# Optimization experiments

Measured on AMD Instinct MI355X. Metric: run time of the kernel, lower is better.

Reference implementation:

```python
import jax, jax.numpy as jnp
import numpy as np

B, S, H, NH = 2, 2048, 2048, 16
HD = H // NH  # 128
ROPE_BASE = 10000.0


def rotate_half(x):
    x1, x2 = x[..., : x.shape[-1] // 2], x[..., x.shape[-1] // 2 :]
    return jnp.concatenate((-x2, x1), axis=-1)


def rope_cos_sin(seq_len, dim, dtype):
    inv_freq = 1.0 / (ROPE_BASE ** (jnp.arange(0, dim, 2, dtype=jnp.float32) / dim))
    t = jnp.arange(seq_len, dtype=jnp.float32)
    freqs = jnp.einsum('i,j->ij', t, inv_freq)          # [S, dim/2]
    emb = jnp.concatenate((freqs, freqs), axis=-1)       # [S, dim]
    return jnp.cos(emb).astype(dtype), jnp.sin(emb).astype(dtype)


def setup_inputs() -> dict:
    key = jax.random.key(0)
    ks = jax.random.split(key, 5)
    std = 1.0 / np.sqrt(H)
    return {
        'hidden_states': jax.random.normal(ks[0], (B, S, H), dtype=jnp.float32),
        'Wq': jax.random.normal(ks[1], (H, H), dtype=jnp.float32) * std,
        'Wk': jax.random.normal(ks[2], (H, H), dtype=jnp.float32) * std,
        'Wv': jax.random.normal(ks[3], (H, H), dtype=jnp.float32) * std,
        'Wo': jax.random.normal(ks[4], (H, H), dtype=jnp.float32) * std,
    }


def reference(hidden_states, Wq, Wk, Wv, Wo):
    bsz, q_len, _ = hidden_states.shape
    scale = 1.0 / np.sqrt(HD)
    # QKV projections (nn.Linear: x @ W.T)
    q = (hidden_states @ Wq.T).reshape(bsz, q_len, NH, HD).transpose(0, 2, 1, 3)
    k = (hidden_states @ Wk.T).reshape(bsz, q_len, NH, HD).transpose(0, 2, 1, 3)
    v = (hidden_states @ Wv.T).reshape(bsz, q_len, NH, HD).transpose(0, 2, 1, 3)
    # RoPE
    cos, sin = rope_cos_sin(q_len, HD, hidden_states.dtype)  # [S, HD]
    cos = cos[None, None]
    sin = sin[None, None]
    q = q * cos + rotate_half(q) * sin
    k = k * cos + rotate_half(k) * sin
    # attention (no mask, eval dropout = identity)
    attn = jnp.einsum('bhqd,bhkd->bhqk', q, k) * scale
    attn = jax.nn.softmax(attn.astype(jnp.float32), axis=-1).astype(q.dtype)
    out = jnp.einsum('bhqk,bhkd->bhqd', attn, v)
    out = out.transpose(0, 2, 1, 3).reshape(bsz, q_len, H)
    return out @ Wo.T
```

## Files before the change

kernel.cpp:

```cpp
#include <hip/hip_runtime.h>
#include <hip/hip_bf16.h>
#include <math.h>

#define Bb 2
#define Ss 2048
#define Hh 2048
#define NHh 16
#define HDd 128
#define Mm (Bb*Ss)

typedef __bf16 bf16;
typedef __bf16 bf16x8 __attribute__((ext_vector_type(8)));
typedef __bf16 bf16x4 __attribute__((ext_vector_type(4)));
typedef float  f32x4  __attribute__((ext_vector_type(4)));

#define MFMA16(a,b,c) __builtin_amdgcn_mfma_f32_16x16x32_bf16((a),(b),(c),0,0,0)

__device__ __forceinline__ void gll16(const void* g, void* l) {
  __builtin_amdgcn_global_load_lds((__attribute__((address_space(1))) void*)g,
                                   (__attribute__((address_space(3))) void*)l, 16, 0, 0);
}

__global__ __launch_bounds__(256) void k_tables(float* __restrict__ cosT, float* __restrict__ sinT) {
  int id = blockIdx.x * 256 + threadIdx.x;
  int s = id >> 6, j = id & 63;
  float inv = 1.0f / powf(10000.0f, (float)j * (1.0f/64.0f));
  float a = (float)s * inv;
  cosT[id] = cosf(a);
  sinT[id] = sinf(a);
}

__global__ __launch_bounds__(256) void k_cvt(const float* __restrict__ in, bf16* __restrict__ out) {
  size_t i = ((size_t)blockIdx.x * 256 + threadIdx.x) * 4;
  float4 v = *(const float4*)(in + i);
  bf16x4 r = { (bf16)v.x, (bf16)v.y, (bf16)v.z, (bf16)v.w };
  *(bf16x4*)(out + i) = r;
}

template<int EPI>
__global__ __launch_bounds__(256) void k_gemm(
    const bf16* __restrict__ A, const bf16* __restrict__ Bw,
    float* __restrict__ C, bf16* __restrict__ QKb, bf16* __restrict__ Vt,
    int M, int N, int K)
{
  __shared__ bf16 As[128*64];
  __shared__ bf16 Bs[128*64];
  const int tid = threadIdx.x;
  const int lane = tid & 63;
  const int w = tid >> 6, wm = w & 1, wn = w >> 1;
  const int cpx = gridDim.x >> 3;
  const int bid = (blockIdx.x & 7) * cpx + (blockIdx.x >> 3);
  const int mt = M >> 7;
  const int bm = bid % mt, bn = bid / mt;
  const int r8 = tid >> 3, c8 = tid & 7;
  const bf16* Ag = A  + (size_t)(bm*128 + r8) * K + c8*8;
  const bf16* Bg = Bw + (size_t)(bn*128 + r8) * K + c8*8;
  bf16* Asw = &As[r8*64 + c8*8];
  bf16* Bsw = &Bs[r8*64 + c8*8];

  f32x4 acc[4][4] = {};
  for (int k0 = 0; k0 < K; k0 += 64) {
#pragma unroll
    for (int i = 0; i < 4; ++i) {
      gll16(Ag + (size_t)i*32*K + k0, Asw + i*32*64);
      gll16(Bg + (size_t)i*32*K + k0, Bsw + i*32*64);
    }
    __syncthreads();
#pragma unroll
    for (int kc = 0; kc < 2; ++kc) {
      bf16x8 af[4], bfv[4];
#pragma unroll
      for (int mi = 0; mi < 4; ++mi)
        af[mi] = *(const bf16x8*)&As[(wm*64 + mi*16 + (lane & 15))*64 + kc*32 + (lane>>4)*8];
#pragma unroll
      for (int ni = 0; ni < 4; ++ni)
        bfv[ni] = *(const bf16x8*)&Bs[(wn*64 + ni*16 + (lane & 15))*64 + kc*32 + (lane>>4)*8];
#pragma unroll
      for (int mi = 0; mi < 4; ++mi)
#pragma unroll
        for (int ni = 0; ni < 4; ++ni)
          acc[mi][ni] = MFMA16(af[mi], bfv[ni], acc[mi][ni]);
    }
    __syncthreads();
  }
  const int colB = bn*128 + wn*64;
  if (EPI == 0) {
#pragma unroll
    for (int mi = 0; mi < 4; ++mi)
#pragma unroll
      for (int ni = 0; ni < 4; ++ni) {
        int row0 = bm*128 + wm*64 + mi*16 + (lane>>4)*4;
        int col  = colB + ni*16 + (lane & 15);
#pragma unroll
        for (int r = 0; r < 4; ++r)
          C[(size_t)(row0 + r) * N + col] = acc[mi][ni][r];
      }
  } else if (colB < 4096) {
#pragma unroll
    for (int mi = 0; mi < 4; ++mi)
#pragma unroll
      for (int ni = 0; ni < 4; ++ni) {
        int row0 = bm*128 + wm*64 + mi*16 + (lane>>4)*4;
        int col  = colB + ni*16 + (lane & 15);
#pragma unroll
        for (int r = 0; r < 4; ++r)
          QKb[(size_t)(row0 + r) * 4096 + col] = (bf16)acc[mi][ni][r];
      }
  } else {
#pragma unroll
    for (int mi = 0; mi < 4; ++mi)
#pragma unroll
      for (int ni = 0; ni < 4; ++ni) {
        int row0 = bm*128 + wm*64 + mi*16 + (lane>>4)*4;
        int n2   = colB + ni*16 + (lane & 15) - 4096;
        int b = row0 >> 11, s0 = row0 & (Ss-1);
        bf16x4 pk = { (bf16)acc[mi][ni][0], (bf16)acc[mi][ni][1],
                      (bf16)acc[mi][ni][2], (bf16)acc[mi][ni][3] };
        *(bf16x4*)&Vt[((size_t)(b*NHh + (n2>>7))*HDd + (n2&127))*Ss + s0] = pk;
      }
  }
}

__global__ __launch_bounds__(256) void k_rope(
    const bf16* __restrict__ QKb,
    const float* __restrict__ cosT, const float* __restrict__ sinT,
    bf16* __restrict__ Qb, bf16* __restrict__ Kb)
{
  const size_t id = (size_t)blockIdx.x * 256 + threadIdx.x;
  const int j = (int)(id & 63);
  const size_t row = id >> 6;
  const size_t tok = row >> 4;
  const int h = (int)(row & 15);
  const int s = (int)(tok & (Ss - 1));
  const float c = cosT[s*64 + j], sn = sinT[s*64 + j];
  const size_t qbase = tok * 4096 + h * 128;
  const float scale = 0.12753102543421936f;
  float q1 = (float)QKb[qbase + j],        q2 = (float)QKb[qbase + 64 + j];
  float k1 = (float)QKb[qbase + 2048 + j], k2 = (float)QKb[qbase + 2048 + 64 + j];
  const size_t obase = row * HDd;
  Qb[obase + j]      = (bf16)((q1*c - q2*sn) * scale);
  Qb[obase + 64 + j] = (bf16)((q2*c + q1*sn) * scale);
  Kb[obase + j]      = (bf16)(k1*c - k2*sn);
  Kb[obase + 64 + j] = (bf16)(k2*c + k1*sn);
}

__global__ __launch_bounds__(256) void k_attn(
    const bf16* __restrict__ Qb, const bf16* __restrict__ Kb,
    const bf16* __restrict__ Vt, bf16* __restrict__ Ob)
{
  __shared__ bf16 Ks[2][64*128];
  __shared__ bf16 Vs[2][128*64];
  __shared__ bf16 Ps[64*72];
  const int cpx = gridDim.x >> 3;
  const int blk = (blockIdx.x & 7) * cpx + (blockIdx.x >> 3);
  const int bh = blk >> 5;
  const int q0 = (blk & 31) * 64;
  const int b = bh >> 4, h = bh & 15;
  const int tid = threadIdx.x, lane = tid & 63, w = tid >> 6;

  const int rK = tid >> 4, cK = tid & 15;
  const int rV = tid >> 3, cV = tid & 7;
  const bf16* Kg0 = Kb + ((size_t)b*Ss*NHh + h) * HDd;
  const bf16* Vg0 = Vt + (size_t)bh * HDd * Ss;

  auto stage = [&](int bufi, int kv0) {
#pragma unroll
    for (int i = 0; i < 4; ++i) {
      const int rowK = i*16 + rK; const int sck = cK ^ (rowK & 7);
      gll16(Kg0 + (size_t)(kv0 + rowK)*(NHh*HDd) + sck*8, &Ks[bufi][rowK*128 + cK*8]);
      const int rowV = i*32 + rV; const int scv = cV ^ (rowV & 7);
      gll16(Vg0 + (size_t)rowV*Ss + kv0 + scv*8, &Vs[bufi][rowV*64 + cV*8]);
    }
  };

  bf16x8 aq[4];
  {
    const int qr = q0 + w*16 + (lane & 15);
    const bf16* qp = Qb + ((size_t)(b*Ss + qr) * NHh + h) * HDd + (lane>>4)*8;
#pragma unroll
    for (int kc = 0; kc < 4; ++kc) aq[kc] = *(const bf16x8*)(qp + kc*32);
  }
  float m_i[4], l_par[4];
  f32x4 o[8] = {};
#pragma unroll
  for (int i = 0; i < 4; ++i) { m_i[i] = -1e30f; l_par[i] = 0.f; }

  stage(0, 0);
  asm volatile("s_waitcnt vmcnt(0)" ::: "memory");
  __builtin_amdgcn_s_barrier();
  asm volatile("" ::: "memory");

  const int NT = Ss / 64;
  for (int t = 0; t < NT; ++t) {
    const int cur = t & 1;
    if (t + 1 < NT) stage(cur ^ 1, (t + 1) * 64);

    f32x4 sf[4];
    __builtin_amdgcn_s_setprio(1);
#pragma unroll
    for (int nf = 0; nf < 4; ++nf) {
      f32x4 a = {0.f,0.f,0.f,0.f};
#pragma unroll
      for (int kc = 0; kc < 4; ++kc) {
        const int row = nf*16 + (lane & 15);
        const int ch  = kc*4 + (lane>>4);
        bf16x8 bk = *(const bf16x8*)&Ks[cur][row*128 + (ch ^ (row & 7))*8];
        a = MFMA16(aq[kc], bk, a);
      }
      sf[nf] = a;
    }
    __builtin_amdgcn_s_setprio(0);

    float xl[4];
#pragma unroll
    for (int i = 0; i < 4; ++i)
      xl[i] = fmaxf(fmaxf(sf[0][i], sf[1][i]), fmaxf(sf[2][i], sf[3][i]));
    bool grow = (xl[0] > m_i[0] + 11.5f) || (xl[1] > m_i[1] + 11.5f) ||
                (xl[2] > m_i[2] + 11.5f) || (xl[3] > m_i[3] + 11.5f);
    if (__any(grow)) {
#pragma unroll
      for (int i = 0; i < 4; ++i) {
        float x = xl[i];
        x = fmaxf(x, __shfl_xor(x, 1));
        x = fmaxf(x, __shfl_xor(x, 2));
        x = fmaxf(x, __shfl_xor(x, 4));
        x = fmaxf(x, __shfl_xor(x, 8));
        float mnew = fmaxf(m_i[i], x);
        float c = exp2f(m_i[i] - mnew);
        m_i[i] = mnew; l_par[i] *= c;
#pragma unroll
        for (int nfo = 0; nfo < 8; ++nfo) o[nfo][i] *= c;
      }
    }
#pragma unroll
    for (int nf = 0; nf < 4; ++nf)
#pragma unroll
      for (int i = 0; i < 4; ++i) {
        float pv = exp2f(sf[nf][i] - m_i[i]);
        sf[nf][i] = pv;
        l_par[i] += pv;
      }
#pragma unroll
    for (int nf = 0; nf < 4; ++nf)
#pragma unroll
      for (int i = 0; i < 4; ++i)
        Ps[(w*16 + (lane>>4)*4 + i)*72 + nf*16 + (lane & 15)] = (bf16)sf[nf][i];

    __builtin_amdgcn_s_setprio(1);
#pragma unroll
    for (int kc = 0; kc < 2; ++kc) {
      bf16x8 pa = *(const bf16x8*)&Ps[(w*16 + (lane & 15))*72 + kc*32 + (lane>>4)*8];
#pragma unroll
      for (int nfo = 0; nfo < 8; ++nfo) {
        const int row = nfo*16 + (lane & 15);
        const int ch  = kc*4 + (lane>>4);
        bf16x8 bv = *(const bf16x8*)&Vs[cur][row*64 + (ch ^ (row & 7))*8];
        o[nfo] = MFMA16(pa, bv, o[nfo]);
      }
    }
    __builtin_amdgcn_s_setprio(0);

    asm volatile("s_waitcnt vmcnt(0)" ::: "memory");
    __builtin_amdgcn_s_barrier();
    asm volatile("" ::: "memory");
  }

  float linv[4];
#pragma unroll
  for (int i = 0; i < 4; ++i) {
    float s = l_par[i];
    s += __shfl_xor(s, 1); s += __shfl_xor(s, 2);
    s += __shfl_xor(s, 4); s += __shfl_xor(s, 8);
    linv[i] = 1.0f / s;
  }
#pragma unroll
  for (int nfo = 0; nfo < 8; ++nfo)
#pragma unroll
    for (int i = 0; i < 4; ++i) {
      const int qr = q0 + w*16 + (lane>>4)*4 + i;
      const int d  = nfo*16 + (lane & 15);
      Ob[((size_t)(b*Ss + qr) * NHh + h) * HDd + d] = (bf16)(o[nfo][i] * linv[i]);
    }
}

extern "C" void kernel_launch(void* const* d_in, const int* in_sizes, int n_in,
                              void* d_out, int out_size, void* d_ws, size_t ws_size,
                              hipStream_t stream) {
  (void)in_sizes; (void)n_in; (void)out_size; (void)ws_size;
  const float* X  = (const float*)d_in[0];
  const float* Wq = (const float*)d_in[1];
  const float* Wk = (const float*)d_in[2];
  const float* Wv = (const float*)d_in[3];
  const float* Wo = (const float*)d_in[4];
  float* out = (float*)d_out;

  char* p = (char*)d_ws;
  size_t off = 0;
  auto take = [&](size_t bytes) { char* r = p + off; off += (bytes + 255) & ~(size_t)255; return r; };

  float* cosT = (float*)take((size_t)Ss*64*4);
  float* sinT = (float*)take((size_t)Ss*64*4);
  bf16*  Xb   = (bf16*) take((size_t)Mm*Hh*2);
  bf16*  Wqkv = (bf16*) take((size_t)3*Hh*Hh*2);
  bf16*  Wob  = (bf16*) take((size_t)Hh*Hh*2);
  bf16*  QKb  = (bf16*) take((size_t)Mm*4096*2);
  bf16*  Vt   = (bf16*) take((size_t)Mm*Hh*2);
  bf16*  Qb   = (bf16*) take((size_t)Mm*Hh*2);
  bf16*  Kb2  = (bf16*) take((size_t)Mm*Hh*2);
  bf16*  Ob   = (bf16*) take((size_t)Mm*Hh*2);

  k_tables<<<(Ss*64)/256, 256, 0, stream>>>(cosT, sinT);
  k_cvt<<<(Mm*Hh)/4/256, 256, 0, stream>>>(X,  Xb);
  k_cvt<<<(Hh*Hh)/4/256, 256, 0, stream>>>(Wq, Wqkv);
  k_cvt<<<(Hh*Hh)/4/256, 256, 0, stream>>>(Wk, Wqkv + (size_t)Hh*Hh);
  k_cvt<<<(Hh*Hh)/4/256, 256, 0, stream>>>(Wv, Wqkv + (size_t)2*Hh*Hh);
  k_cvt<<<(Hh*Hh)/4/256, 256, 0, stream>>>(Wo, Wob);

  k_gemm<1><<<(Mm/128) * (3*Hh/128), 256, 0, stream>>>(Xb, Wqkv, nullptr, QKb, Vt, Mm, 3*Hh, Hh);
  k_rope<<<((size_t)Mm*NHh*64)/256, 256, 0, stream>>>(QKb, cosT, sinT, Qb, Kb2);
  k_attn<<<Bb*NHh*(Ss/64), 256, 0, stream>>>(Qb, Kb2, Vt, Ob);
  k_gemm<0><<<(Mm/128) * (Hh/128), 256, 0, stream>>>(Ob, Wob, out, nullptr, nullptr, Mm, Hh, Hh);
}
```

Measured before the change: 501.8 us.

## Add 256x256 double-buffered 8-wave QKV GEMM with swizzled LDS and interleaved prefetch

```diff
diff --git a/kernel.cpp b/kernel.cpp
--- a/kernel.cpp
+++ b/kernel.cpp
@@ -37,11 +37,136 @@
   *(bf16x4*)(out + i) = r;
 }
 
-template<int EPI>
-__global__ __launch_bounds__(256) void k_gemm(
+__global__ __launch_bounds__(512, 2) void k_gemm8_qkv(
     const bf16* __restrict__ A, const bf16* __restrict__ Bw,
-    float* __restrict__ C, bf16* __restrict__ QKb, bf16* __restrict__ Vt,
-    int M, int N, int K)
+    bf16* __restrict__ QKb, bf16* __restrict__ Vt)
+{
+  constexpr int K = Hh;
+  constexpr int NT = K / 64;
+  constexpr int NITER = NT / 2;
+  __shared__ bf16 As[2][16384];
+  __shared__ bf16 Bs[2][16384];
+  const int tid = threadIdx.x;
+  const int lane = tid & 63;
+  const int w = tid >> 6;
+  const int wm = w >> 2, wn = w & 3;
+  const int l15 = lane & 15, l4 = lane >> 4;
+  const int cpx = gridDim.x >> 3;
+  const int bid = (blockIdx.x & 7) * cpx + (blockIdx.x >> 3);
+  const int bm = bid & 15, bn = bid >> 4;
+
+  auto stageHalf = [&](int d, int isB, int half, int kt) {
+    const bf16* g = isB ? Bw : A;
+    const int rowbase = (isB ? bn : bm) * 256 + half * 128;
+    bf16* lb = isB ? &Bs[d][half*8192] : &As[d][half*8192];
+#pragma unroll
+    for (int issue = 0; issue < 2; ++issue) {
+      int slot = issue*512 + tid;
+      int r = slot >> 3, c = slot & 7;
+      int cs = c ^ (r & 7);
+      gll16(g + (size_t)(rowbase + r) * K + kt*64 + cs*8, lb + slot*8);
+    }
+  };
+
+  f32x4 acc[8][4] = {};
+  bf16x8 bfr[4][2];
+
+  stageHalf(0,0,0,0); stageHalf(0,0,1,0);
+  stageHalf(0,1,0,0); stageHalf(0,1,1,0);
+  stageHalf(1,1,0,1); stageHalf(1,1,1,1);
+  asm volatile("s_waitcnt vmcnt(0)" ::: "memory");
+  __builtin_amdgcn_s_barrier();
+
+  for (int it = 0; it < NITER; ++it) {
+    const int more = (it < NITER-1);
+    const int kt1 = 2*it+1, kt2 = 2*it+2, kt3 = 2*it+3;
+#pragma unroll
+    for (int hp = 0; hp < 2; ++hp) {
+#pragma unroll
+      for (int q = 0; q < 4; ++q) {
+        if (q == 0) {
+#pragma unroll
+          for (int nf = 0; nf < 4; ++nf)
+#pragma unroll
+            for (int kc = 0; kc < 2; ++kc) {
+              int row = wn*64 + nf*16 + l15;
+              int ch  = kc*4 + l4;
+              bfr[nf][kc] = *(const bf16x8*)&Bs[hp][row*64 + ((ch ^ (row & 7))*8)];
+            }
+        }
+        bf16x8 afr[2][2];
+#pragma unroll
+        for (int i = 0; i < 2; ++i)
+#pragma unroll
+          for (int kc = 0; kc < 2; ++kc) {
+            int row = wm*128 + (q*2+i)*16 + l15;
+            int ch  = kc*4 + l4;
+            afr[i][kc] = *(const bf16x8*)&As[hp][row*64 + ((ch ^ (row & 7))*8)];
+          }
+        const int ph = hp*4 + q;
+        if      (ph == 0)      stageHalf(1,0,0,kt1);
+        else if (ph == 1)      stageHalf(1,0,1,kt1);
+        else if (more) {
+          if      (ph == 2)    stageHalf(0,1,0,kt2);
+          else if (ph == 3)    stageHalf(0,1,1,kt2);
+          else if (ph == 4)    stageHalf(0,0,0,kt2);
+          else if (ph == 5)    stageHalf(0,0,1,kt2);
+          else if (ph == 6)    stageHalf(1,1,0,kt3);
+          else                 stageHalf(1,1,1,kt3);
+        }
+        __builtin_amdgcn_s_barrier();
+        __builtin_amdgcn_s_setprio(1);
+#pragma unroll
+        for (int i = 0; i < 2; ++i)
+#pragma unroll
+          for (int nf = 0; nf < 4; ++nf)
+#pragma unroll
+            for (int kc = 0; kc < 2; ++kc)
+              acc[q*2+i][nf] = MFMA16(afr[i][kc], bfr[nf][kc], acc[q*2+i][nf]);
+        __builtin_amdgcn_s_setprio(0);
+        asm volatile("s_waitcnt lgkmcnt(0)" ::: "memory");
+        __builtin_amdgcn_sched_barrier(0);
+        if (ph == 3) {
+          if (more) asm volatile("s_waitcnt vmcnt(4)" ::: "memory");
+          else      asm volatile("s_waitcnt vmcnt(0)" ::: "memory");
+        } else if (ph == 7 && more) {
+          asm volatile("s_waitcnt vmcnt(4)" ::: "memory");
+        }
+        __builtin_amdgcn_s_barrier();
+      }
+    }
+  }
+
+  const int col0 = bn*256;
+  if (col0 < 4096) {
+#pragma unroll
+    for (int mf = 0; mf < 8; ++mf)
+#pragma unroll
+      for (int nf = 0; nf < 4; ++nf) {
+        int row0 = bm*256 + wm*128 + mf*16 + l4*4;
+        int col  = col0 + wn*64 + nf*16 + l15;
+#pragma unroll
+        for (int r = 0; r < 4; ++r)
+          QKb[(size_t)(row0 + r) * 4096 + col] = (bf16)acc[mf][nf][r];
+      }
+  } else {
+#pragma unroll
+    for (int mf = 0; mf < 8; ++mf)
+#pragma unroll
+      for (int nf = 0; nf < 4; ++nf) {
+        int row0 = bm*256 + wm*128 + mf*16 + l4*4;
+        int n2   = col0 + wn*64 + nf*16 + l15 - 4096;
+        int b = row0 >> 11, s0 = row0 & (Ss-1);
+        bf16x4 pk = { (bf16)acc[mf][nf][0], (bf16)acc[mf][nf][1],
+                      (bf16)acc[mf][nf][2], (bf16)acc[mf][nf][3] };
+        *(bf16x4*)&Vt[((size_t)(b*NHh + (n2>>7))*HDd + (n2&127))*Ss + s0] = pk;
+      }
+  }
+}
+
+__global__ __launch_bounds__(256) void k_gemm_f32(
+    const bf16* __restrict__ A, const bf16* __restrict__ Bw,
+    float* __restrict__ C, int M, int N, int K)
 {
   __shared__ bf16 As[128*64];
   __shared__ bf16 Bs[128*64];
@@ -83,42 +208,16 @@
     }
     __syncthreads();
   }
-  const int colB = bn*128 + wn*64;
-  if (EPI == 0) {
-#pragma unroll
-    for (int mi = 0; mi < 4; ++mi)
-#pragma unroll
-      for (int ni = 0; ni < 4; ++ni) {
-        int row0 = bm*128 + wm*64 + mi*16 + (lane>>4)*4;
-        int col  = colB + ni*16 + (lane & 15);
-#pragma unroll
-        for (int r = 0; r < 4; ++r)
-          C[(size_t)(row0 + r) * N + col] = acc[mi][ni][r];
-      }
-  } else if (colB < 4096) {
-#pragma unroll
-    for (int mi = 0; mi < 4; ++mi)
-#pragma unroll
-      for (int ni = 0; ni < 4; ++ni) {
-        int row0 = bm*128 + wm*64 + mi*16 + (lane>>4)*4;
-        int col  = colB + ni*16 + (lane & 15);
-#pragma unroll
-        for (int r = 0; r < 4; ++r)
-          QKb[(size_t)(row0 + r) * 4096 + col] = (bf16)acc[mi][ni][r];
-      }
-  } else {
-#pragma unroll
-    for (int mi = 0; mi < 4; ++mi)
-#pragma unroll
-      for (int ni = 0; ni < 4; ++ni) {
-        int row0 = bm*128 + wm*64 + mi*16 + (lane>>4)*4;
-        int n2   = colB + ni*16 + (lane & 15) - 4096;
-        int b = row0 >> 11, s0 = row0 & (Ss-1);
-        bf16x4 pk = { (bf16)acc[mi][ni][0], (bf16)acc[mi][ni][1],
-                      (bf16)acc[mi][ni][2], (bf16)acc[mi][ni][3] };
-        *(bf16x4*)&Vt[((size_t)(b*NHh + (n2>>7))*HDd + (n2&127))*Ss + s0] = pk;
-      }
-  }
+#pragma unroll
+  for (int mi = 0; mi < 4; ++mi)
+#pragma unroll
+    for (int ni = 0; ni < 4; ++ni) {
+      int row0 = bm*128 + wm*64 + mi*16 + (lane>>4)*4;
+      int col  = bn*128 + wn*64 + ni*16 + (lane & 15);
+#pragma unroll
+      for (int r = 0; r < 4; ++r)
+        C[(size_t)(row0 + r) * N + col] = acc[mi][ni][r];
+    }
 }
 
 __global__ __launch_bounds__(256) void k_rope(
@@ -316,8 +415,8 @@
   k_cvt<<<(Hh*Hh)/4/256, 256, 0, stream>>>(Wv, Wqkv + (size_t)2*Hh*Hh);
   k_cvt<<<(Hh*Hh)/4/256, 256, 0, stream>>>(Wo, Wob);
 
-  k_gemm<1><<<(Mm/128) * (3*Hh/128), 256, 0, stream>>>(Xb, Wqkv, nullptr, QKb, Vt, Mm, 3*Hh, Hh);
+  k_gemm8_qkv<<<(Mm/256) * (3*Hh/256), 512, 0, stream>>>(Xb, Wqkv, QKb, Vt);
   k_rope<<<((size_t)Mm*NHh*64)/256, 256, 0, stream>>>(QKb, cosT, sinT, Qb, Kb2);
   k_attn<<<Bb*NHh*(Ss/64), 256, 0, stream>>>(Qb, Kb2, Vt, Ob);
-  k_gemm<0><<<(Mm/128) * (Hh/128), 256, 0, stream>>>(Ob, Wob, out, nullptr, nullptr, Mm, Hh, Hh);
-}
+  k_gemm_f32<<<(Mm/128) * (Hh/128), 256, 0, stream>>>(Ob, Wob, out, Mm, Hh, Hh);
+}
```

Result: faster. 465.9 us (-7.2%).
